# Performance work log

Measured on AMD Instinct MI355X. Metric: run time of the kernel, lower is better.

Reference implementation:

```python
import jax, jax.numpy as jnp
import numpy as np

DIM = 512
NUM_HEADS = 8
HEAD_DIM = DIM // NUM_HEADS
SCALE = HEAD_DIM ** -0.5


def setup_inputs() -> dict:
    key = jax.random.key(0)
    kx, kqw, kqb, kpw, kpb = jax.random.split(key, 5)
    B, N = 2, 4096
    x = jax.random.normal(kx, (B, N, DIM), dtype=jnp.float32)
    # nn.Linear weights stored as [out, in]; init ~ U(-1/sqrt(in), 1/sqrt(in))
    bound = 1.0 / np.sqrt(DIM)
    qkv_w = jax.random.uniform(kqw, (3 * DIM, DIM), minval=-bound, maxval=bound, dtype=jnp.float32)
    qkv_b = jax.random.uniform(kqb, (3 * DIM,), minval=-bound, maxval=bound, dtype=jnp.float32)
    proj_w = jax.random.uniform(kpw, (DIM, DIM), minval=-bound, maxval=bound, dtype=jnp.float32)
    proj_b = jax.random.uniform(kpb, (DIM,), minval=-bound, maxval=bound, dtype=jnp.float32)
    return {"x": x, "qkv_w": qkv_w, "qkv_b": qkv_b, "proj_w": proj_w, "proj_b": proj_b}


def reference(x, qkv_w, qkv_b, proj_w, proj_b):
    B, N, C = x.shape
    # qkv: [B, N, 3C] -> [3, B, H, N, Dh]
    qkv = x @ qkv_w.T + qkv_b
    qkv = qkv.reshape(B, N, 3, NUM_HEADS, HEAD_DIM).transpose(2, 0, 3, 1, 4)
    q, k, v = qkv[0], qkv[1], qkv[2]
    # scores: [B, H, N, N] (materialized, matching the original math)
    attn = jnp.einsum("bhqd,bhkd->bhqk", q, k) * SCALE
    attn = jax.nn.softmax(attn, axis=-1)
    out = jnp.einsum("bhqk,bhkd->bhqd", attn, v)  # [B, H, N, Dh]
    out = out.transpose(0, 2, 1, 3).reshape(B, N, C)
    return out @ proj_w.T + proj_b
```

## Files before the change

kernel.cpp:

```cpp
#include <hip/hip_runtime.h>
#include <hip/hip_bf16.h>
#include <stdint.h>
#include <stddef.h>

typedef __attribute__((ext_vector_type(8))) short short8;
typedef __attribute__((ext_vector_type(4))) float f32x4;
typedef __attribute__((ext_vector_type(16))) float f32x16;

#define MFMA16(a, b, c) __builtin_amdgcn_mfma_f32_16x16x32_bf16((a), (b), (c), 0, 0, 0)
#define MFMA32(a, b, c) __builtin_amdgcn_mfma_f32_32x32x16_bf16((a), (b), (c), 0, 0, 0)

#define QSCALE 0.1803368801111204f

#if __has_builtin(__builtin_amdgcn_exp2f)
#define EXP2(x) __builtin_amdgcn_exp2f(x)
#else
#define EXP2(x) __builtin_exp2f(x)
#endif

__device__ __forceinline__ float b2f(short x) {
    unsigned u = ((unsigned)(unsigned short)x) << 16;
    float f; __builtin_memcpy(&f, &u, 4); return f;
}
__device__ __forceinline__ short f2b(float f) {
    unsigned u; __builtin_memcpy(&u, &f, 4);
    u = (u + 0x7FFFu + ((u >> 16) & 1u)) >> 16;
    return (short)u;
}
__device__ __forceinline__ unsigned pack2(float a, float b) {
    unsigned ua, ub; __builtin_memcpy(&ua, &a, 4); __builtin_memcpy(&ub, &b, 4);
    return __builtin_amdgcn_perm(ub + 0x8000u, ua + 0x8000u, 0x07060302u);
}
__device__ __forceinline__ unsigned cvtpk(float a, float b) {
    unsigned r;
    asm("v_cvt_pk_bf16_f32 %0, %1, %2" : "=v"(r) : "v"(a), "v"(b));
    return r;
}
__device__ __forceinline__ short8 load8f(const float* p) {
    const float4 f0 = *(const float4*)p;
    const float4 f1 = *(const float4*)(p + 4);
    short8 r;
    r[0]=f2b(f0.x); r[1]=f2b(f0.y); r[2]=f2b(f0.z); r[3]=f2b(f0.w);
    r[4]=f2b(f1.x); r[5]=f2b(f1.y); r[6]=f2b(f1.z); r[7]=f2b(f1.w);
    return r;
}

__global__ __launch_bounds__(256) void cvt3(
    const float* __restrict__ s0, short* __restrict__ d0, int n0,
    const float* __restrict__ s1, short* __restrict__ d1, int n1,
    const float* __restrict__ s2, short* __restrict__ d2, int n2)
{
    int i = blockIdx.x * 256 + threadIdx.x;
    if (i < n0) { *(short8*)(d0 + (size_t)i * 8) = load8f(s0 + (size_t)i * 8); return; }
    i -= n0;
    if (i < n1) { *(short8*)(d1 + (size_t)i * 8) = load8f(s1 + (size_t)i * 8); return; }
    i -= n1;
    if (i < n2) { *(short8*)(d2 + (size_t)i * 8) = load8f(s2 + (size_t)i * 8); }
}

__global__ __launch_bounds__(256) void qkv_gemm(
    const short* __restrict__ X, const short* __restrict__ W,
    const float* __restrict__ bias,
    short* __restrict__ Qb, short* __restrict__ Kb, short* __restrict__ Vb)
{
    __shared__ short sT[128][132];

    const int tid  = threadIdx.x;
    const int wv   = tid >> 6;
    const int lane = tid & 63;
    const int l15  = lane & 15;
    const int quad = lane >> 4;
    const int m0   = blockIdx.x * 128 + (wv >> 1) * 64;
    const int sec  = blockIdx.y >> 2;
    const int bis  = blockIdx.y & 3;
    const int nbase = sec * 512 + bis * 128;
    const int j0   = (wv & 1) * 64;

    const f32x4 zero = {0.f, 0.f, 0.f, 0.f};
    f32x4 acc[4][4];
#pragma unroll
    for (int i = 0; i < 4; i++)
#pragma unroll
        for (int j = 0; j < 4; j++) acc[i][j] = zero;

    for (int k0 = 0; k0 < 512; k0 += 32) {
        short8 a[4], b[4];
#pragma unroll
        for (int i = 0; i < 4; i++)
            a[i] = *(const short8*)(X + (size_t)(m0 + i * 16 + l15) * 512 + k0 + quad * 8);
#pragma unroll
        for (int j = 0; j < 4; j++)
            b[j] = *(const short8*)(W + (size_t)(nbase + j0 + j * 16 + l15) * 512 + k0 + quad * 8);
#pragma unroll
        for (int i = 0; i < 4; i++)
#pragma unroll
            for (int j = 0; j < 4; j++)
                acc[i][j] = MFMA16(a[i], b[j], acc[i][j]);
    }

    if (sec < 2) {
        const float scale = (sec == 0) ? QSCALE : 1.0f;
        short* dst = (sec == 0) ? Qb : Kb;
#pragma unroll
        for (int j = 0; j < 4; j++) {
            const int jc = bis * 128 + j0 + j * 16 + l15;
            const float bs = bias[sec * 512 + jc];
            const int hl = jc >> 6, d = jc & 63;
#pragma unroll
            for (int i = 0; i < 4; i++) {
#pragma unroll
                for (int r = 0; r < 4; r++) {
                    const int m = m0 + i * 16 + quad * 4 + r;
                    const int bb = m >> 12, seq = m & 4095;
                    dst[((size_t)(bb * 8 + hl) * 4096 + seq) * 64 + d] =
                        f2b((acc[i][j][r] + bs) * scale);
                }
            }
        }
    } else {
#pragma unroll
        for (int j = 0; j < 4; j++) {
            const int jcl = j0 + j * 16 + l15;
            const float bs = bias[nbase + jcl];
#pragma unroll
            for (int i = 0; i < 4; i++) {
                uint2 w;
                w.x = pack2(acc[i][j][0] + bs, acc[i][j][1] + bs);
                w.y = pack2(acc[i][j][2] + bs, acc[i][j][3] + bs);
                *(uint2*)&sT[jcl][(wv >> 1) * 64 + i * 16 + quad * 4] = w;
            }
        }
        __syncthreads();

        const int jcl = tid >> 1, half = tid & 1;
        const int hl = (bis * 128 + jcl) >> 6;
        const int d  = jcl & 63;
        const int bb = (blockIdx.x * 128) >> 12;
        const int seq0 = ((blockIdx.x * 128) & 4095) + half * 64;
        short* dst = Vb + ((size_t)(bb * 8 + hl) * 64 + d) * 4096 + seq0;
#pragma unroll
        for (int u = 0; u < 8; u++)
            *(short8*)(dst + u * 8) = *(const short8*)&sT[jcl][half * 64 + u * 8];
    }
}

__global__ __launch_bounds__(512, 4) void flash_attn(
    const short* __restrict__ Q, const short* __restrict__ K,
    const short* __restrict__ V, short* __restrict__ PO0,
    short* __restrict__ PO1, float* __restrict__ lbuf, int niter)
{
    __shared__ short sK[2][128][72];
    __shared__ short sV[2][64][136];

    const int tid  = threadIdx.x;
    const int wv   = tid >> 6;
    const int lane = tid & 63;
    const int l31  = lane & 31;
    const int half = lane >> 5;
    const int bh = blockIdx.y;
    const int b = bh >> 3, h = bh & 7;
    const int qw = blockIdx.x * 256 + wv * 32;
    const int ks = blockIdx.z;
    const int key0 = ks * niter * 128;

    const short* Qb = Q + (size_t)bh * 4096 * 64;
    const short* Kb = K + (size_t)bh * 4096 * 64;
    const short* Vb = V + (size_t)bh * 64 * 4096;

    short8 aq[4];
#pragma unroll
    for (int s = 0; s < 4; s++)
        aq[s] = *(const short8*)(Qb + (size_t)(qw + l31) * 64 + s * 16 + half * 8);

    short8 ones;
#pragma unroll
    for (int j = 0; j < 8; j++) ones[j] = (short)0x3F80;

    f32x16 o0 = {}, o1 = {};
    f32x16 o2 = {};

    const int r0  = tid >> 3;
    const int scb = (tid & 7) * 8;
    const int vb  = (scb & ~12) | ((scb & 8) >> 1);

    short8 pk0, pk1, pv0, pv1;
    pk0 = *(const short8*)(Kb + (size_t)(key0 + r0) * 64 + scb);
    pk1 = *(const short8*)(Kb + (size_t)(key0 + 64 + r0) * 64 + scb);
    pv0 = *(const short8*)(Vb + (size_t)r0 * 4096 + key0 + scb);
    pv1 = *(const short8*)(Vb + (size_t)r0 * 4096 + key0 + 64 + scb);
    *(short8*)&sK[0][r0][scb]      = pk0;
    *(short8*)&sK[0][64 + r0][scb] = pk1;
    *(uint2*)&sV[0][r0][vb]          = ((const uint2*)&pv0)[0];
    *(uint2*)&sV[0][r0][vb + 8]      = ((const uint2*)&pv0)[1];
    *(uint2*)&sV[0][r0][64 + vb]     = ((const uint2*)&pv1)[0];
    *(uint2*)&sV[0][r0][64 + vb + 8] = ((const uint2*)&pv1)[1];
    {
        const int kn = key0 + 128;
        pk0 = *(const short8*)(Kb + (size_t)(kn + r0) * 64 + scb);
        pk1 = *(const short8*)(Kb + (size_t)(kn + 64 + r0) * 64 + scb);
        pv0 = *(const short8*)(Vb + (size_t)r0 * 4096 + kn + scb);
        pv1 = *(const short8*)(Vb + (size_t)r0 * 4096 + kn + 64 + scb);
    }

    for (int kt = 0; kt < niter; ++kt) {
        __syncthreads();

        if (kt + 1 < niter) {
            short (*sKn)[72]  = sK[(kt + 1) & 1];
            short (*sVn)[136] = sV[(kt + 1) & 1];
            *(short8*)&sKn[r0][scb]      = pk0;
            *(short8*)&sKn[64 + r0][scb] = pk1;
            *(uint2*)&sVn[r0][vb]          = ((const uint2*)&pv0)[0];
            *(uint2*)&sVn[r0][vb + 8]      = ((const uint2*)&pv0)[1];
            *(uint2*)&sVn[r0][64 + vb]     = ((const uint2*)&pv1)[0];
            *(uint2*)&sVn[r0][64 + vb + 8] = ((const uint2*)&pv1)[1];
        }
        if (kt + 2 < niter) {
            const int kn = key0 + (kt + 2) * 128;
            pk0 = *(const short8*)(Kb + (size_t)(kn + r0) * 64 + scb);
            pk1 = *(const short8*)(Kb + (size_t)(kn + 64 + r0) * 64 + scb);
            pv0 = *(const short8*)(Vb + (size_t)r0 * 4096 + kn + scb);
            pv1 = *(const short8*)(Vb + (size_t)r0 * 4096 + kn + 64 + scb);
        }

        const short (*sKc)[72]  = sK[kt & 1];
        const short (*sVc)[136] = sV[kt & 1];

#pragma unroll
        for (int i = 0; i < 4; i++) {
            const int c = (i + wv) & 3;
            f32x16 ST = {};
            __builtin_amdgcn_s_setprio(1);
#pragma unroll
            for (int s = 0; s < 4; s++) {
                const short8 bk = *(const short8*)&sKc[c * 32 + l31][s * 16 + half * 8];
                ST = MFMA32(bk, aq[s], ST);
            }
            __builtin_amdgcn_s_setprio(0);
            float e[16];
#pragma unroll
            for (int r = 0; r < 16; r++) e[r] = EXP2(ST[r]);
            uint4 w0 = { cvtpk(e[0], e[1]),   cvtpk(e[2], e[3]),
                         cvtpk(e[4], e[5]),   cvtpk(e[6], e[7]) };
            uint4 w1 = { cvtpk(e[8], e[9]),   cvtpk(e[10], e[11]),
                         cvtpk(e[12], e[13]), cvtpk(e[14], e[15]) };
            const short8 bp0 = *(const short8*)&w0;
            const short8 bp1 = *(const short8*)&w1;

            __builtin_amdgcn_s_setprio(1);
            const short8 bv00 = *(const short8*)&sVc[l31][(2 * c) * 16 + half * 8];
            const short8 bv01 = *(const short8*)&sVc[32 + l31][(2 * c) * 16 + half * 8];
            o0 = MFMA32(bv00, bp0, o0);
            o1 = MFMA32(bv01, bp0, o1);
            o2 = MFMA32(ones, bp0, o2);
            const short8 bv10 = *(const short8*)&sVc[l31][(2 * c + 1) * 16 + half * 8];
            const short8 bv11 = *(const short8*)&sVc[32 + l31][(2 * c + 1) * 16 + half * 8];
            o0 = MFMA32(bv10, bp1, o0);
            o1 = MFMA32(bv11, bp1, o1);
            o2 = MFMA32(ones, bp1, o2);
            __builtin_amdgcn_s_setprio(0);
        }
    }

    const float lsum = o2[0];
    const float inv = 1.f / fmaxf(lsum, 1e-30f);

    short* PO = (ks == 0) ? PO0 : PO1;
#pragma unroll
    for (int q = 0; q < 4; q++) {
        uint2 w0, w1;
        w0.x = pack2(o0[4 * q + 0] * inv, o0[4 * q + 1] * inv);
        w0.y = pack2(o0[4 * q + 2] * inv, o0[4 * q + 3] * inv);
        w1.x = pack2(o1[4 * q + 0] * inv, o1[4 * q + 1] * inv);
        w1.y = pack2(o1[4 * q + 2] * inv, o1[4 * q + 3] * inv);
        const size_t rowoff = ((size_t)b * 4096 + qw + l31) * 512;
        const int col = h * 64 + q * 8 + half * 4;
        *(uint2*)(PO + rowoff + col) = w0;
        *(uint2*)(PO + rowoff + col + 32) = w1;
    }
    if (half == 0)
        lbuf[((size_t)ks * 16 + bh) * 4096 + qw + l31] = lsum;
}

__global__ __launch_bounds__(256) void combine(
    const short* __restrict__ PO0, const short* __restrict__ PO1,
    short* __restrict__ attn, const float* __restrict__ L)
{
    const int i = blockIdx.x * 256 + threadIdx.x;
    const size_t flat = (size_t)i * 8;
    const int col = (int)(flat & 511);
    const int q   = (int)((flat >> 9) & 4095);
    const int b   = (int)(flat >> 21);
    const int bh  = b * 8 + (col >> 6);
    const float l0 = L[(size_t)bh * 4096 + q];
    const float l1 = L[(size_t)65536 + (size_t)bh * 4096 + q];
    const float inv = 1.f / (l0 + l1);
    const float w0 = l0 * inv, w1 = l1 * inv;
    const short8 a = *(const short8*)(PO0 + flat);
    const short8 c = *(const short8*)(PO1 + flat);
    short8 r;
#pragma unroll
    for (int k = 0; k < 8; k += 2) {
        const unsigned p = pack2(w0 * b2f(a[k]) + w1 * b2f(c[k]),
                                 w0 * b2f(a[k + 1]) + w1 * b2f(c[k + 1]));
        r[k]     = (short)(p & 0xFFFF);
        r[k + 1] = (short)(p >> 16);
    }
    *(short8*)(attn + flat) = r;
}

__global__ __launch_bounds__(256) void proj_gemm(
    const short* __restrict__ A, const short* __restrict__ W,
    const float* __restrict__ bias, float* __restrict__ dst)
{
    const int tid  = threadIdx.x;
    const int wv   = tid >> 6;
    const int lane = tid & 63;
    const int l15  = lane & 15;
    const int quad = lane >> 4;
    const int m0 = blockIdx.x * 128 + (wv >> 1) * 64;
    const int n0 = blockIdx.y * 128 + (wv & 1) * 64;

    const f32x4 zero = {0.f, 0.f, 0.f, 0.f};
    f32x4 acc[4][4];
#pragma unroll
    for (int i = 0; i < 4; i++)
#pragma unroll
        for (int j = 0; j < 4; j++) acc[i][j] = zero;

    for (int k0 = 0; k0 < 512; k0 += 32) {
        short8 a[4], b[4];
#pragma unroll
        for (int i = 0; i < 4; i++)
            a[i] = *(const short8*)(A + (size_t)(m0 + i * 16 + l15) * 512 + k0 + quad * 8);
#pragma unroll
        for (int j = 0; j < 4; j++)
            b[j] = *(const short8*)(W + (size_t)(n0 + j * 16 + l15) * 512 + k0 + quad * 8);
#pragma unroll
        for (int i = 0; i < 4; i++)
#pragma unroll
            for (int j = 0; j < 4; j++)
                acc[i][j] = MFMA16(a[i], b[j], acc[i][j]);
    }

#pragma unroll
    for (int j = 0; j < 4; j++) {
        const int n = n0 + j * 16 + l15;
        const float bs = bias[n];
#pragma unroll
        for (int i = 0; i < 4; i++) {
#pragma unroll
            for (int r = 0; r < 4; r++) {
                const int m = m0 + i * 16 + quad * 4 + r;
                dst[(size_t)m * 512 + n] = acc[i][j][r] + bs;
            }
        }
    }
}

extern "C" void kernel_launch(void* const* d_in, const int* in_sizes, int n_in,
                              void* d_out, int out_size, void* d_ws, size_t ws_size,
                              hipStream_t stream)
{
    const float* x      = (const float*)d_in[0];
    const float* qkv_w  = (const float*)d_in[1];
    const float* qkv_b  = (const float*)d_in[2];
    const float* proj_w = (const float*)d_in[3];
    const float* proj_b = (const float*)d_in[4];

    const size_t MB = 1024 * 1024;
    short* xb   = (short*)d_out;
    short* wb   = (short*)d_out + 4 * MB;
    short* PO0  = (short*)d_out;
    short* PO1  = (short*)d_out + 4 * MB;
    float* out  = (float*)d_out;

    short* Qf = (short*)d_ws;
    short* Kf = Qf + (size_t)16 * 4096 * 64;
    short* Vf = Kf + (size_t)16 * 4096 * 64;
    short* attn = Qf;
    float* lbuf = (float*)((char*)d_ws + 24 * MB);
    short* pwb  = (short*)((char*)d_ws + 24 * MB + 512 * 1024);

    cvt3<<<2560, 256, 0, stream>>>(x, xb, 524288, qkv_w, wb, 98304, proj_w, pwb, 32768);
    qkv_gemm<<<dim3(64, 12), 256, 0, stream>>>(xb, wb, qkv_b, Qf, Kf, Vf);
    flash_attn<<<dim3(16, 16, 2), 512, 0, stream>>>(Qf, Kf, Vf, PO0, PO1, lbuf, 16);
    combine<<<2048, 256, 0, stream>>>(PO0, PO1, attn, lbuf);
    proj_gemm<<<dim3(64, 4), 256, 0, stream>>>(attn, pwb, proj_b, out);
}
```

Before: 246.8 us.

## Compute softmax row sums with VALU adds and coalesce Q/K stores via LDS

```diff
diff --git a/kernel.cpp b/kernel.cpp
--- a/kernel.cpp
+++ b/kernel.cpp
@@ -103,20 +103,27 @@
         short* dst = (sec == 0) ? Qb : Kb;
 #pragma unroll
         for (int j = 0; j < 4; j++) {
-            const int jc = bis * 128 + j0 + j * 16 + l15;
-            const float bs = bias[sec * 512 + jc];
-            const int hl = jc >> 6, d = jc & 63;
+            const int jcl = j0 + j * 16 + l15;
+            const float bs = bias[sec * 512 + bis * 128 + jcl];
 #pragma unroll
             for (int i = 0; i < 4; i++) {
-#pragma unroll
-                for (int r = 0; r < 4; r++) {
-                    const int m = m0 + i * 16 + quad * 4 + r;
-                    const int bb = m >> 12, seq = m & 4095;
-                    dst[((size_t)(bb * 8 + hl) * 4096 + seq) * 64 + d] =
-                        f2b((acc[i][j][r] + bs) * scale);
-                }
+                const int s0 = (wv >> 1) * 64 + i * 16 + quad * 4;
+#pragma unroll
+                for (int r = 0; r < 4; r++)
+                    sT[s0 + r][jcl] = f2b((acc[i][j][r] + bs) * scale);
             }
         }
+        __syncthreads();
+
+        const int seqlocal = tid & 127;
+        const int hl_loc   = tid >> 7;
+        const int hl  = bis * 2 + hl_loc;
+        const int m   = blockIdx.x * 128 + seqlocal;
+        const int bb  = m >> 12, seqg = m & 4095;
+        short* drow = dst + ((size_t)(bb * 8 + hl) * 4096 + seqg) * 64;
+#pragma unroll
+        for (int u = 0; u < 8; u++)
+            *(short8*)(drow + u * 8) = *(const short8*)&sT[seqlocal][hl_loc * 64 + u * 8];
     } else {
 #pragma unroll
         for (int j = 0; j < 4; j++) {
@@ -172,12 +179,8 @@
     for (int s = 0; s < 4; s++)
         aq[s] = *(const short8*)(Qb + (size_t)(qw + l31) * 64 + s * 16 + half * 8);
 
-    short8 ones;
-#pragma unroll
-    for (int j = 0; j < 8; j++) ones[j] = (short)0x3F80;
-
     f32x16 o0 = {}, o1 = {};
-    f32x16 o2 = {};
+    float la0 = 0.f, la1 = 0.f, la2 = 0.f, la3 = 0.f;
 
     const int r0  = tid >> 3;
     const int scb = (tid & 7) * 8;
@@ -240,6 +243,10 @@
             float e[16];
 #pragma unroll
             for (int r = 0; r < 16; r++) e[r] = EXP2(ST[r]);
+            la0 += (e[0] + e[1]) + (e[2] + e[3]);
+            la1 += (e[4] + e[5]) + (e[6] + e[7]);
+            la2 += (e[8] + e[9]) + (e[10] + e[11]);
+            la3 += (e[12] + e[13]) + (e[14] + e[15]);
             uint4 w0 = { cvtpk(e[0], e[1]),   cvtpk(e[2], e[3]),
                          cvtpk(e[4], e[5]),   cvtpk(e[6], e[7]) };
             uint4 w1 = { cvtpk(e[8], e[9]),   cvtpk(e[10], e[11]),
@@ -252,17 +259,16 @@
             const short8 bv01 = *(const short8*)&sVc[32 + l31][(2 * c) * 16 + half * 8];
             o0 = MFMA32(bv00, bp0, o0);
             o1 = MFMA32(bv01, bp0, o1);
-            o2 = MFMA32(ones, bp0, o2);
             const short8 bv10 = *(const short8*)&sVc[l31][(2 * c + 1) * 16 + half * 8];
             const short8 bv11 = *(const short8*)&sVc[32 + l31][(2 * c + 1) * 16 + half * 8];
             o0 = MFMA32(bv10, bp1, o0);
             o1 = MFMA32(bv11, bp1, o1);
-            o2 = MFMA32(ones, bp1, o2);
             __builtin_amdgcn_s_setprio(0);
         }
     }
 
-    const float lsum = o2[0];
+    float lsum = (la0 + la1) + (la2 + la3);
+    lsum += __shfl_xor(lsum, 32);
     const float inv = 1.f / fmaxf(lsum, 1e-30f);
 
     short* PO = (ks == 0) ? PO0 : PO1;
```

After: 230.6 us. 1.07x faster.
